# Kernel optimization log

Measured on AMD Instinct MI355X. Metric: run time of the kernel, lower is better.

## Reference

```python
import jax, jax.numpy as jnp
import numpy as np
from jax import lax

N, H, W, CIN = 64, 256, 256, 3   # batch, image HxW, RGB
C, K = 32, 5                     # cross-conv channels / kernel size (from reshape(-1,32,5,5))
ADIM, AHID = 4, 256              # action dim, action-encoder hidden


def _conv(x, w, b, stride, pad):
    # x [N,C,H,W], w [O,I,kh,kw] (torch OIHW cross-correlation semantics)
    y = lax.conv_general_dilated(x, w, (stride, stride), [(pad, pad), (pad, pad)],
                                 dimension_numbers=('NCHW', 'OIHW', 'NCHW'))
    return y + b[None, :, None, None]


def cross_convolve(feat, kernels):
    # feat [N,C,h,w], kernels [N,C,K,K]; per-sample per-channel 'same' conv (padding=2).
    # Equivalent to the original N*C loop of tiny F.conv2d calls: one depthwise
    # (grouped, feature_group_count=C) conv per sample, vmapped over the batch.
    def one(x, k):  # x [C,h,w], k [C,K,K]
        y = lax.conv_general_dilated(x[None], k[:, None], (1, 1), [(2, 2), (2, 2)],
                                     dimension_numbers=('NCHW', 'OIHW', 'NCHW'),
                                     feature_group_count=C)
        return y[0]
    return jax.vmap(one)(feat, kernels)


def setup_inputs() -> dict:
    key = jax.random.key(0)
    ks = jax.random.split(key, 10)
    g = lambda i, shape, s: jax.random.normal(ks[i], shape, jnp.float32) * s
    return {
        'images': jax.random.normal(ks[0], (N, H, W, CIN), jnp.float32),
        'actions': jax.random.normal(ks[1], (N, ADIM), jnp.float32),
        # phys_encoder: conv(3->32,k5,s2,p2) relu, conv(32->32,k5,s2,p2) relu
        'pe_w1': g(2, (C, CIN, 5, 5), 0.08), 'pe_b1': jnp.zeros((C,), jnp.float32),
        'pe_w2': g(3, (C, C, 5, 5), 0.04), 'pe_b2': jnp.zeros((C,), jnp.float32),
        # action_encoder MLP: ADIM -> AHID -> C*K*K (=800)
        'ae_w1': g(4, (ADIM, AHID), 0.3), 'ae_b1': jnp.zeros((AHID,), jnp.float32),
        'ae_w2': g(5, (AHID, C * K * K), 0.05), 'ae_b2': jnp.zeros((C * K * K,), jnp.float32),
        # motion_predictor: conv(32->32,k3,p1) relu, conv(32->2,k3,p1)
        'mp_w1': g(6, (C, C, 3, 3), 0.06), 'mp_b1': jnp.zeros((C,), jnp.float32),
        'mp_w2': g(7, (2, C, 3, 3), 0.06), 'mp_b2': jnp.zeros((2,), jnp.float32),
    }


def reference(images, actions, pe_w1, pe_b1, pe_w2, pe_b2,
              ae_w1, ae_b1, ae_w2, ae_b2, mp_w1, mp_b1, mp_w2, mp_b2):
    x = jnp.transpose(images, (0, 3, 1, 2))                 # NHWC -> NCHW
    h = jax.nn.relu(_conv(x, pe_w1, pe_b1, 2, 2))           # [N,32,128,128]
    h = jax.nn.relu(_conv(h, pe_w2, pe_b2, 2, 2))           # [N,32,64,64]
    a = jax.nn.relu(actions @ ae_w1 + ae_b1)
    a = (a @ ae_w2 + ae_b2).reshape(-1, C, K, K)            # per-sample kernels [N,32,5,5]
    sa = cross_convolve(h, a)                               # [N,32,64,64]
    f = jax.nn.relu(_conv(sa, mp_w1, mp_b1, 1, 1))
    flow = _conv(f, mp_w2, mp_b2, 1, 1)                     # [N,2,64,64]
    return flow
```

## Files before the change

kernel.cpp:

```cpp
#include <hip/hip_runtime.h>


typedef __attribute__((ext_vector_type(8))) short bf16x8;
typedef __attribute__((ext_vector_type(4))) float f32x4;

__device__ __forceinline__ unsigned short f2bf(float f) {
    unsigned int u = __float_as_uint(f);
    u = (u + 0x7FFFu + ((u >> 16) & 1u)) >> 16;
    return (unsigned short)u;
}
__device__ __forceinline__ float bf2f(unsigned short h) {
    return __uint_as_float(((unsigned int)h) << 16);
}

__global__ __launch_bounds__(64) void zero_border_kernel(unsigned int* t, int R, int pad) {
    int row = blockIdx.x % R;
    int n   = blockIdx.x / R;
    int tid = threadIdx.x;
    unsigned int* rp = t + (size_t)(n * R + row) * R * 16;
    if (row < pad || row >= R - pad) {
        for (int i = tid; i < R * 16; i += 64) rp[i] = 0u;
    } else {
        for (int i = tid; i < pad * 16; i += 64) {
            rp[i] = 0u;
            rp[(size_t)(R - pad) * 16 + i] = 0u;
        }
    }
}

__global__ __launch_bounds__(256) void pad_img_kernel(const float* __restrict__ img,
                                                      unsigned short* __restrict__ imgp) {
    const int py = blockIdx.x % 260;
    const int n  = blockIdx.x / 260;
    const int iy = py - 2;
    const bool rowok = (iy >= 0) && (iy < 256);
    const float* srow = img + ((size_t)n * 256 + (rowok ? iy : 0)) * 768;
    unsigned short* drow = imgp + (size_t)(n * 260 + py) * 1056;
    for (int s = threadIdx.x; s < 1056; s += 256) {
        int px = s >> 2, c = s & 3;
        int ix = px - 2;
        float v = 0.f;
        if (rowok && c < 3 && ix >= 0 && ix < 256) v = srow[ix * 3 + c];
        drow[s] = f2bf(v);
    }
}

__global__ __launch_bounds__(256) void repack_conv1b(const float* __restrict__ src, unsigned short* __restrict__ dst) {
    int idx = blockIdx.x * 256 + threadIdx.x;
    if (idx >= 5120) return;
    int kh = idx / 1024, r = idx % 1024, o = r / 32, k = r % 32, dx = k >> 2, c = k & 3;
    float v = (dx < 5 && c < 3) ? src[o * 75 + c * 25 + kh * 5 + dx] : 0.f;
    dst[idx] = f2bf(v);
}
__global__ __launch_bounds__(256) void repack_conv2(const float* __restrict__ src, unsigned short* __restrict__ dst) {
    int idx = blockIdx.x * 256 + threadIdx.x;
    if (idx >= 25600) return;
    int co = idx / 800, r = idx % 800, ci = r / 25, tap = r % 25;
    dst[(tap * 32 + co) * 32 + ci] = f2bf(src[idx]);
}
__global__ __launch_bounds__(256) void repack_mp1(const float* __restrict__ src, unsigned short* __restrict__ dst) {
    int idx = blockIdx.x * 256 + threadIdx.x;
    if (idx >= 9216) return;
    int co = idx / 288, r = idx % 288, ci = r / 9, tap = r % 9;
    dst[(tap * 32 + co) * 32 + ci] = f2bf(src[idx]);
}
__global__ __launch_bounds__(256) void repack_mp2b(const float* __restrict__ src, unsigned short* __restrict__ dst) {
    int idx = blockIdx.x * 256 + threadIdx.x;
    if (idx >= 4608) return;
    int tap = idx / 512, r = idx % 512, co = r / 32, ci = r % 32;
    float v = (co < 2) ? src[co * 288 + ci * 9 + tap] : 0.f;
    dst[idx] = f2bf(v);
}

__global__ __launch_bounds__(256) void mlp_kernel(const float* __restrict__ actions,
                                                  const float* __restrict__ w1,
                                                  const float* __restrict__ b1,
                                                  const float* __restrict__ w2,
                                                  const float* __restrict__ b2,
                                                  float* __restrict__ aout) {
    int n = blockIdx.y;
    int t = threadIdx.x;
    __shared__ float hid[256];
    float a0 = actions[n * 4 + 0], a1 = actions[n * 4 + 1];
    float a2 = actions[n * 4 + 2], a3 = actions[n * 4 + 3];
    float acc = b1[t];
    acc += a0 * w1[0 * 256 + t] + a1 * w1[1 * 256 + t] +
           a2 * w1[2 * 256 + t] + a3 * w1[3 * 256 + t];
    hid[t] = fmaxf(acc, 0.0f);
    __syncthreads();
    int o = blockIdx.x * 200 + t;
    if (t < 200) {
        float s = b2[o];
        #pragma unroll 4
        for (int i = 0; i < 256; ++i) s += hid[i] * w2[i * 800 + o];
        aout[n * 800 + o] = s;
    }
}

__global__ __launch_bounds__(256) void conv1_mfma(const unsigned short* __restrict__ imgp,
                                                  const short* __restrict__ B1,
                                                  const float* __restrict__ bias,
                                                  unsigned short* __restrict__ h1p) {
    const int tid = threadIdx.x;
    const int lane = tid & 63;
    const int w = tid >> 6;
    const int n = blockIdx.y;
    const int cohalf = w & 1;
    const int oy = blockIdx.x * 2 + (w >> 1);
    const int ml = lane & 15;
    const int kg = lane >> 4;

    bf16x8 bfrag[5];
    #pragma unroll
    for (int kh = 0; kh < 5; ++kh)
        bfrag[kh] = *(const bf16x8*)(B1 + ((kh * 32 + cohalf * 16 + ml) * 32 + kg * 8));
    const float bia = bias[cohalf * 16 + ml];
    const int co = cohalf * 16 + ml;

    f32x4 acc[8];
    #pragma unroll
    for (int t = 0; t < 8; ++t) acc[t] = (f32x4){bia, bia, bia, bia};

    #pragma unroll
    for (int kh = 0; kh < 5; ++kh) {
        const unsigned short* rowbase = imgp + (size_t)(n * 260 + 2 * oy + kh) * 1056;
        #pragma unroll
        for (int t = 0; t < 8; ++t) {
            const int px0 = 2 * (16 * t + ml) + 2 * kg;
            bf16x8 af = *(const bf16x8*)(rowbase + px0 * 4);
            acc[t] = __builtin_amdgcn_mfma_f32_16x16x32_bf16(af, bfrag[kh], acc[t], 0, 0, 0);
        }
    }
    #pragma unroll
    for (int t = 0; t < 8; ++t) {
        #pragma unroll
        for (int r = 0; r < 4; ++r) {
            const int px = 16 * t + kg * 4 + r;
            h1p[((size_t)(n * 132 + oy + 2) * 132 + px + 2) * 32 + co] = f2bf(fmaxf(acc[t][r], 0.f));
        }
    }
}

__global__ __launch_bounds__(256) void conv2_mfma(const unsigned short* __restrict__ h1p,
                                                  const short* __restrict__ B,
                                                  const float* __restrict__ bias,
                                                  unsigned short* __restrict__ h2p) {
    const int tid = threadIdx.x;
    const int lane = tid & 63;
    const int w = tid >> 6;
    const int n = blockIdx.y;
    const int cohalf = w & 1;
    const int ml = lane & 15;
    const int kg = lane >> 4;

    bf16x8 bfrag[25];
    #pragma unroll
    for (int t = 0; t < 25; ++t)
        bfrag[t] = *(const bf16x8*)(B + ((t * 32 + cohalf * 16 + ml) * 32 + kg * 8));
    const float bia = bias[cohalf * 16 + ml];
    const int co = cohalf * 16 + ml;

    for (int it = 0; it < 2; ++it) {
        const int oy = blockIdx.x * 4 + (w >> 1) * 2 + it;
        f32x4 acc[4];
        #pragma unroll
        for (int t = 0; t < 4; ++t) acc[t] = (f32x4){bia, bia, bia, bia};
        #pragma unroll
        for (int kh = 0; kh < 5; ++kh) {
            const unsigned short* rowbase = h1p + (size_t)(n * 132 + 2 * oy + kh) * (132 * 32);
            #pragma unroll
            for (int kw = 0; kw < 5; ++kw) {
                bf16x8 af[4];
                #pragma unroll
                for (int t = 0; t < 4; ++t) {
                    const int ixp = 2 * (16 * t + ml) + kw;
                    af[t] = *(const bf16x8*)(rowbase + ixp * 32 + kg * 8);
                }
                const int tap = kh * 5 + kw;
                #pragma unroll
                for (int t = 0; t < 4; ++t)
                    acc[t] = __builtin_amdgcn_mfma_f32_16x16x32_bf16(af[t], bfrag[tap], acc[t], 0, 0, 0);
            }
        }
        #pragma unroll
        for (int t = 0; t < 4; ++t) {
            #pragma unroll
            for (int r = 0; r < 4; ++r) {
                const int px = 16 * t + kg * 4 + r;
                h2p[((size_t)(n * 68 + oy + 2) * 68 + px + 2) * 32 + co] = f2bf(fmaxf(acc[t][r], 0.f));
            }
        }
    }
}

__global__ __launch_bounds__(256) void xconv_kernel(const unsigned short* __restrict__ h2p,
                                                    const float* __restrict__ ker,
                                                    unsigned short* __restrict__ sap) {
    __shared__ __align__(16) unsigned short tile[12 * 68 * 32];
    const int tid = threadIdx.x;
    const int n = blockIdx.x;
    const int rb = blockIdx.y;
    const unsigned short* src = h2p + (size_t)(n * 68 + rb * 8) * (68 * 32);
    for (int i = tid; i < 3264; i += 256)
        *(uint4*)(tile + i * 8) = *(const uint4*)(src + i * 8);
    const int ci = tid & 31, xg = tid >> 5;
    const float* kp = ker + (size_t)(n * 32 + ci) * 25;
    float k[25];
    #pragma unroll
    for (int t = 0; t < 25; ++t) k[t] = kp[t];
    __syncthreads();

    float acc[8][8];
    #pragma unroll
    for (int r = 0; r < 8; ++r)
        #pragma unroll
        for (int j = 0; j < 8; ++j) acc[r][j] = 0.f;

    #pragma unroll
    for (int ir = 0; ir < 12; ++ir) {
        float v[12];
        #pragma unroll
        for (int t = 0; t < 12; ++t)
            v[t] = bf2f(tile[(ir * 68 + xg * 8 + t) * 32 + ci]);
        #pragma unroll
        for (int kh = 0; kh < 5; ++kh) {
            const int r = ir - kh;
            if (r >= 0 && r < 8) {
                #pragma unroll
                for (int j = 0; j < 8; ++j) {
                    float s = acc[r][j];
                    #pragma unroll
                    for (int kw = 0; kw < 5; ++kw) s += k[kh * 5 + kw] * v[j + kw];
                    acc[r][j] = s;
                }
            }
        }
    }
    #pragma unroll
    for (int r = 0; r < 8; ++r)
        #pragma unroll
        for (int j = 0; j < 8; ++j)
            sap[((size_t)(n * 66 + rb * 8 + r + 1) * 66 + xg * 8 + j + 1) * 32 + ci] = f2bf(acc[r][j]);
}

__global__ __launch_bounds__(256) void mp1_mfma(const unsigned short* __restrict__ sap,
                                                const short* __restrict__ B,
                                                const float* __restrict__ bias,
                                                unsigned short* __restrict__ fp) {
    const int tid = threadIdx.x;
    const int lane = tid & 63;
    const int w = tid >> 6;
    const int n = blockIdx.y;
    const int cohalf = w & 1;
    const int ml = lane & 15;
    const int kg = lane >> 4;

    bf16x8 bfrag[9];
    #pragma unroll
    for (int t = 0; t < 9; ++t)
        bfrag[t] = *(const bf16x8*)(B + ((t * 32 + cohalf * 16 + ml) * 32 + kg * 8));
    const float bia = bias[cohalf * 16 + ml];
    const int co = cohalf * 16 + ml;

    for (int it = 0; it < 2; ++it) {
        const int oy = blockIdx.x * 4 + (w >> 1) * 2 + it;
        f32x4 acc[4];
        #pragma unroll
        for (int t = 0; t < 4; ++t) acc[t] = (f32x4){bia, bia, bia, bia};
        #pragma unroll
        for (int kh = 0; kh < 3; ++kh) {
            const unsigned short* rowbase = sap + (size_t)(n * 66 + oy + kh) * (66 * 32);
            #pragma unroll
            for (int kw = 0; kw < 3; ++kw) {
                bf16x8 af[4];
                #pragma unroll
                for (int t = 0; t < 4; ++t)
                    af[t] = *(const bf16x8*)(rowbase + (16 * t + ml + kw) * 32 + kg * 8);
                #pragma unroll
                for (int t = 0; t < 4; ++t)
                    acc[t] = __builtin_amdgcn_mfma_f32_16x16x32_bf16(af[t], bfrag[kh * 3 + kw], acc[t], 0, 0, 0);
            }
        }
        #pragma unroll
        for (int t = 0; t < 4; ++t) {
            #pragma unroll
            for (int r = 0; r < 4; ++r) {
                const int px = 16 * t + kg * 4 + r;
                fp[((size_t)(n * 66 + oy + 1) * 66 + px + 1) * 32 + co] = f2bf(fmaxf(acc[t][r], 0.f));
            }
        }
    }
}

__global__ __launch_bounds__(256) void mp2_mfma(const unsigned short* __restrict__ fpb,
                                                const short* __restrict__ B,
                                                const float* __restrict__ bias,
                                                float* __restrict__ out) {
    const int tid = threadIdx.x;
    const int lane = tid & 63;
    const int w = tid >> 6;
    const int n = blockIdx.y;
    const int oy = blockIdx.x * 4 + w;
    const int ml = lane & 15;
    const int kg = lane >> 4;

    bf16x8 bfrag[9];
    #pragma unroll
    for (int t = 0; t < 9; ++t)
        bfrag[t] = *(const bf16x8*)(B + ((t * 16 + ml) * 32 + kg * 8));
    const float bia = (ml < 2) ? bias[ml] : 0.f;

    f32x4 acc[4];
    #pragma unroll
    for (int t = 0; t < 4; ++t) acc[t] = (f32x4){bia, bia, bia, bia};

    #pragma unroll
    for (int kh = 0; kh < 3; ++kh) {
        const unsigned short* rowbase = fpb + (size_t)(n * 66 + oy + kh) * (66 * 32);
        #pragma unroll
        for (int kw = 0; kw < 3; ++kw) {
            #pragma unroll
            for (int t = 0; t < 4; ++t) {
                bf16x8 af = *(const bf16x8*)(rowbase + (16 * t + ml + kw) * 32 + kg * 8);
                acc[t] = __builtin_amdgcn_mfma_f32_16x16x32_bf16(af, bfrag[kh * 3 + kw], acc[t], 0, 0, 0);
            }
        }
    }
    if (ml < 2) {
        #pragma unroll
        for (int t = 0; t < 4; ++t) {
            #pragma unroll
            for (int r = 0; r < 4; ++r) {
                const int px = 16 * t + kg * 4 + r;
                out[(size_t)n * 8192 + (size_t)ml * 4096 + (size_t)oy * 64 + px] = acc[t][r];
            }
        }
    }
}

extern "C" void kernel_launch(void* const* d_in, const int* in_sizes, int n_in,
                              void* d_out, int out_size, void* d_ws, size_t ws_size,
                              hipStream_t stream) {
    (void)in_sizes; (void)n_in; (void)out_size; (void)ws_size;
    const float* images  = (const float*)d_in[0];
    const float* actions = (const float*)d_in[1];
    const float* pe_w1   = (const float*)d_in[2];
    const float* pe_b1   = (const float*)d_in[3];
    const float* pe_w2   = (const float*)d_in[4];
    const float* pe_b2   = (const float*)d_in[5];
    const float* ae_w1   = (const float*)d_in[6];
    const float* ae_b1   = (const float*)d_in[7];
    const float* ae_w2   = (const float*)d_in[8];
    const float* ae_b2   = (const float*)d_in[9];
    const float* mp_w1   = (const float*)d_in[10];
    const float* mp_b1   = (const float*)d_in[11];
    const float* mp_w2   = (const float*)d_in[12];
    const float* mp_b2   = (const float*)d_in[13];
    float* out = (float*)d_out;

    char* ws = (char*)d_ws;
    float* a_ker          = (float*)(ws + 0);
    unsigned short* B1    = (unsigned short*)(ws + 204800);
    unsigned short* B2    = (unsigned short*)(ws + 215040);
    unsigned short* Bm1   = (unsigned short*)(ws + 266240);
    unsigned short* Bm2   = (unsigned short*)(ws + 284672);
    unsigned short* h1p   = (unsigned short*)(ws + 524288);
    unsigned short* imgp  = (unsigned short*)(ws + 71892992);
    unsigned short* h2p   = (unsigned short*)(ws + 71892992);
    unsigned short* sap   = (unsigned short*)(ws + 90832896);
    unsigned short* fpb   = (unsigned short*)(ws + 108675072);

    repack_conv1b<<<20, 256, 0, stream>>>(pe_w1, B1);
    repack_conv2<<<100, 256, 0, stream>>>(pe_w2, B2);
    repack_mp1<<<36, 256, 0, stream>>>(mp_w1, Bm1);
    repack_mp2b<<<18, 256, 0, stream>>>(mp_w2, Bm2);
    mlp_kernel<<<dim3(4, 64), 256, 0, stream>>>(actions, ae_w1, ae_b1, ae_w2, ae_b2, a_ker);

    zero_border_kernel<<<64 * 132, 64, 0, stream>>>((unsigned int*)h1p, 132, 2);
    zero_border_kernel<<<64 * 66, 64, 0, stream>>>((unsigned int*)fpb, 66, 1);

    pad_img_kernel<<<64 * 260, 256, 0, stream>>>(images, imgp);
    conv1_mfma<<<dim3(64, 64), 256, 0, stream>>>(imgp, (const short*)B1, pe_b1, h1p);

    zero_border_kernel<<<64 * 68, 64, 0, stream>>>((unsigned int*)h2p, 68, 2);
    zero_border_kernel<<<64 * 66, 64, 0, stream>>>((unsigned int*)sap, 66, 1);

    conv2_mfma<<<dim3(16, 64), 256, 0, stream>>>(h1p, (const short*)B2, pe_b2, h2p);
    xconv_kernel<<<dim3(64, 8), 256, 0, stream>>>(h2p, a_ker, sap);
    mp1_mfma<<<dim3(16, 64), 256, 0, stream>>>(sap, (const short*)Bm1, mp_b1, fpb);
    mp2_mfma<<<dim3(16, 64), 256, 0, stream>>>(fpb, (const short*)Bm2, mp_b2, out);
}
```

Measured before the change: 341.3 us.

## Switch conv2 and mp1 to 32x32x16 MFMA with LDS-staged weights

Rewrites the conv2 and first motion-predictor convolutions to use 32x32x16 bf16 MFMA tiles. Each wave now computes a 32-pixel by 32-channel output tile, with weights staged in padded shared memory instead of held in registers. Grids double and each wave handles one output row. This aims to cut register pressure, raise occupancy and improve MFMA efficiency, at the cost of extra LDS traffic and per-kh barriers in conv2.

```diff
diff --git a/kernel.cpp b/kernel.cpp
--- a/kernel.cpp
+++ b/kernel.cpp
@@ -3,6 +3,7 @@
 
 typedef __attribute__((ext_vector_type(8))) short bf16x8;
 typedef __attribute__((ext_vector_type(4))) float f32x4;
+typedef __attribute__((ext_vector_type(16))) float f32x16;
 
 __device__ __forceinline__ unsigned short f2bf(float f) {
     unsigned int u = __float_as_uint(f);
@@ -141,55 +142,54 @@
     }
 }
 
-__global__ __launch_bounds__(256) void conv2_mfma(const unsigned short* __restrict__ h1p,
-                                                  const short* __restrict__ B,
-                                                  const float* __restrict__ bias,
-                                                  unsigned short* __restrict__ h2p) {
+__global__ __launch_bounds__(256, 6) void conv2_mfma32(const unsigned short* __restrict__ h1p,
+                                                       const unsigned int* __restrict__ B,
+                                                       const float* __restrict__ bias,
+                                                       unsigned short* __restrict__ h2p) {
+    __shared__ unsigned int Bs[5 * 32 * 20];
     const int tid = threadIdx.x;
     const int lane = tid & 63;
     const int w = tid >> 6;
     const int n = blockIdx.y;
-    const int cohalf = w & 1;
-    const int ml = lane & 15;
-    const int kg = lane >> 4;
-
-    bf16x8 bfrag[25];
-    #pragma unroll
-    for (int t = 0; t < 25; ++t)
-        bfrag[t] = *(const bf16x8*)(B + ((t * 32 + cohalf * 16 + ml) * 32 + kg * 8));
-    const float bia = bias[cohalf * 16 + ml];
-    const int co = cohalf * 16 + ml;
-
-    for (int it = 0; it < 2; ++it) {
-        const int oy = blockIdx.x * 4 + (w >> 1) * 2 + it;
-        f32x4 acc[4];
-        #pragma unroll
-        for (int t = 0; t < 4; ++t) acc[t] = (f32x4){bia, bia, bia, bia};
-        #pragma unroll
-        for (int kh = 0; kh < 5; ++kh) {
-            const unsigned short* rowbase = h1p + (size_t)(n * 132 + 2 * oy + kh) * (132 * 32);
-            #pragma unroll
-            for (int kw = 0; kw < 5; ++kw) {
-                bf16x8 af[4];
-                #pragma unroll
-                for (int t = 0; t < 4; ++t) {
-                    const int ixp = 2 * (16 * t + ml) + kw;
-                    af[t] = *(const bf16x8*)(rowbase + ixp * 32 + kg * 8);
-                }
-                const int tap = kh * 5 + kw;
-                #pragma unroll
-                for (int t = 0; t < 4; ++t)
-                    acc[t] = __builtin_amdgcn_mfma_f32_16x16x32_bf16(af[t], bfrag[tap], acc[t], 0, 0, 0);
-            }
-        }
-        #pragma unroll
-        for (int t = 0; t < 4; ++t) {
-            #pragma unroll
-            for (int r = 0; r < 4; ++r) {
-                const int px = 16 * t + kg * 4 + r;
-                h2p[((size_t)(n * 68 + oy + 2) * 68 + px + 2) * 32 + co] = f2bf(fmaxf(acc[t][r], 0.f));
-            }
-        }
+    const int oy = blockIdx.x * 2 + (w >> 1);
+    const int x0 = (w & 1) * 32;
+    const int co = lane & 31;
+    const int kgrp = lane >> 5;
+
+    const float bia = bias[co];
+    f32x16 acc;
+    #pragma unroll
+    for (int r = 0; r < 16; ++r) acc[r] = bia;
+
+    const unsigned short* bbase = (const unsigned short*)Bs + co * 40 + kgrp * 8;
+    const int px0 = 2 * (x0 + co);
+
+    for (int kh = 0; kh < 5; ++kh) {
+        if (kh) __syncthreads();
+        const unsigned int* src = B + kh * 2560;
+        #pragma unroll
+        for (int i = tid; i < 2560; i += 256) {
+            int row = i >> 4, p = i & 15;
+            Bs[row * 20 + p] = src[i];
+        }
+        __syncthreads();
+
+        const unsigned short* rowbase = h1p + (size_t)(n * 132 + 2 * oy + kh) * (132 * 32) + kgrp * 8;
+        #pragma unroll
+        for (int kw = 0; kw < 5; ++kw) {
+            bf16x8 a0 = *(const bf16x8*)(rowbase + (px0 + kw) * 32);
+            bf16x8 a1 = *(const bf16x8*)(rowbase + (px0 + kw) * 32 + 16);
+            bf16x8 b0 = *(const bf16x8*)(bbase + kw * (32 * 40));
+            bf16x8 b1 = *(const bf16x8*)(bbase + kw * (32 * 40) + 16);
+            acc = __builtin_amdgcn_mfma_f32_32x32x16_bf16(a0, b0, acc, 0, 0, 0);
+            acc = __builtin_amdgcn_mfma_f32_32x32x16_bf16(a1, b1, acc, 0, 0, 0);
+        }
+    }
+    #pragma unroll
+    for (int r = 0; r < 16; ++r) {
+        const int px = (r & 3) + 8 * (r >> 2) + 4 * kgrp;
+        const int ox = x0 + px;
+        h2p[((size_t)(n * 68 + oy + 2) * 68 + ox + 2) * 32 + co] = f2bf(fmaxf(acc[r], 0.f));
     }
 }
 
@@ -243,52 +243,54 @@
             sap[((size_t)(n * 66 + rb * 8 + r + 1) * 66 + xg * 8 + j + 1) * 32 + ci] = f2bf(acc[r][j]);
 }
 
-__global__ __launch_bounds__(256) void mp1_mfma(const unsigned short* __restrict__ sap,
-                                                const short* __restrict__ B,
-                                                const float* __restrict__ bias,
-                                                unsigned short* __restrict__ fp) {
-    const int tid = threadIdx.x;
+__global__ __launch_bounds__(256, 6) void mp1_mfma32(const unsigned short* __restrict__ sap,
+                                                     const unsigned int* __restrict__ B,
+                                                     const float* __restrict__ bias,
+                                                     unsigned short* __restrict__ fp) {
+    __shared__ unsigned int Bs[9 * 32 * 20];
+    const int tid = threadIdx.x;
+    #pragma unroll
+    for (int i = tid; i < 4608; i += 256) {
+        int row = i >> 4, p = i & 15;
+        Bs[row * 20 + p] = B[i];
+    }
+    __syncthreads();
+
     const int lane = tid & 63;
     const int w = tid >> 6;
     const int n = blockIdx.y;
-    const int cohalf = w & 1;
-    const int ml = lane & 15;
-    const int kg = lane >> 4;
-
-    bf16x8 bfrag[9];
-    #pragma unroll
-    for (int t = 0; t < 9; ++t)
-        bfrag[t] = *(const bf16x8*)(B + ((t * 32 + cohalf * 16 + ml) * 32 + kg * 8));
-    const float bia = bias[cohalf * 16 + ml];
-    const int co = cohalf * 16 + ml;
-
-    for (int it = 0; it < 2; ++it) {
-        const int oy = blockIdx.x * 4 + (w >> 1) * 2 + it;
-        f32x4 acc[4];
-        #pragma unroll
-        for (int t = 0; t < 4; ++t) acc[t] = (f32x4){bia, bia, bia, bia};
-        #pragma unroll
-        for (int kh = 0; kh < 3; ++kh) {
-            const unsigned short* rowbase = sap + (size_t)(n * 66 + oy + kh) * (66 * 32);
-            #pragma unroll
-            for (int kw = 0; kw < 3; ++kw) {
-                bf16x8 af[4];
-                #pragma unroll
-                for (int t = 0; t < 4; ++t)
-                    af[t] = *(const bf16x8*)(rowbase + (16 * t + ml + kw) * 32 + kg * 8);
-                #pragma unroll
-                for (int t = 0; t < 4; ++t)
-                    acc[t] = __builtin_amdgcn_mfma_f32_16x16x32_bf16(af[t], bfrag[kh * 3 + kw], acc[t], 0, 0, 0);
-            }
-        }
-        #pragma unroll
-        for (int t = 0; t < 4; ++t) {
-            #pragma unroll
-            for (int r = 0; r < 4; ++r) {
-                const int px = 16 * t + kg * 4 + r;
-                fp[((size_t)(n * 66 + oy + 1) * 66 + px + 1) * 32 + co] = f2bf(fmaxf(acc[t][r], 0.f));
-            }
-        }
+    const int oy = blockIdx.x * 2 + (w >> 1);
+    const int x0 = (w & 1) * 32;
+    const int co = lane & 31;
+    const int kgrp = lane >> 5;
+
+    const float bia = bias[co];
+    f32x16 acc;
+    #pragma unroll
+    for (int r = 0; r < 16; ++r) acc[r] = bia;
+
+    const unsigned short* bbase = (const unsigned short*)Bs + co * 40 + kgrp * 8;
+    const int px0 = x0 + co;
+
+    #pragma unroll
+    for (int kh = 0; kh < 3; ++kh) {
+        const unsigned short* rowbase = sap + (size_t)(n * 66 + oy + kh) * (66 * 32) + kgrp * 8;
+        #pragma unroll
+        for (int kw = 0; kw < 3; ++kw) {
+            const int tap = kh * 3 + kw;
+            bf16x8 a0 = *(const bf16x8*)(rowbase + (px0 + kw) * 32);
+            bf16x8 a1 = *(const bf16x8*)(rowbase + (px0 + kw) * 32 + 16);
+            bf16x8 b0 = *(const bf16x8*)(bbase + tap * (32 * 40));
+            bf16x8 b1 = *(const bf16x8*)(bbase + tap * (32 * 40) + 16);
+            acc = __builtin_amdgcn_mfma_f32_32x32x16_bf16(a0, b0, acc, 0, 0, 0);
+            acc = __builtin_amdgcn_mfma_f32_32x32x16_bf16(a1, b1, acc, 0, 0, 0);
+        }
+    }
+    #pragma unroll
+    for (int r = 0; r < 16; ++r) {
+        const int px = (r & 3) + 8 * (r >> 2) + 4 * kgrp;
+        const int ox = x0 + px;
+        fp[((size_t)(n * 66 + oy + 1) * 66 + ox + 1) * 32 + co] = f2bf(fmaxf(acc[r], 0.f));
     }
 }
 
@@ -385,8 +387,8 @@
     zero_border_kernel<<<64 * 68, 64, 0, stream>>>((unsigned int*)h2p, 68, 2);
     zero_border_kernel<<<64 * 66, 64, 0, stream>>>((unsigned int*)sap, 66, 1);
 
-    conv2_mfma<<<dim3(16, 64), 256, 0, stream>>>(h1p, (const short*)B2, pe_b2, h2p);
+    conv2_mfma32<<<dim3(32, 64), 256, 0, stream>>>(h1p, (const unsigned int*)B2, pe_b2, h2p);
     xconv_kernel<<<dim3(64, 8), 256, 0, stream>>>(h2p, a_ker, sap);
-    mp1_mfma<<<dim3(16, 64), 256, 0, stream>>>(sap, (const short*)Bm1, mp_b1, fpb);
+    mp1_mfma32<<<dim3(32, 64), 256, 0, stream>>>(sap, (const unsigned int*)Bm1, mp_b1, fpb);
     mp2_mfma<<<dim3(16, 64), 256, 0, stream>>>(fpb, (const short*)Bm2, mp_b2, out);
 }
```

Result: faster. 296.1 us (-13.2%).
